# Performance work log

Hardware: AMD Instinct MI355X
Metric: run time of the kernel (lower is better)

## Reference

```python
import jax, jax.numpy as jnp
import numpy as np

N_NODES = 50000
N_EDGES = 800000
DIM = 128
N_LAYERS = 4
EPS = 1e-5  # BatchNorm1d default eps


def setup_inputs() -> dict:
    key = jax.random.key(0)
    k_x, k_e, k_w = jax.random.split(key, 3)
    x = jax.random.normal(k_x, (N_NODES, DIM), dtype=jnp.float32)
    edge_index = jax.random.randint(k_e, (2, N_EDGES), 0, N_NODES, dtype=jnp.int32)
    # stacked per-layer params (input_dim == hidden_dim == DIM)
    Ws = jax.random.normal(k_w, (N_LAYERS, DIM, DIM), dtype=jnp.float32) * (1.0 / np.sqrt(DIM))
    bs = jnp.zeros((N_LAYERS, DIM), jnp.float32)
    gammas = jnp.ones((N_LAYERS, DIM), jnp.float32)
    betas = jnp.zeros((N_LAYERS, DIM), jnp.float32)
    return {"x": x, "edge_index": edge_index, "Ws": Ws, "bs": bs,
            "gammas": gammas, "betas": betas}


def gcn_conv(x, W, b, src, dst, n):
    # PyG GCNConv: h = X W; out = D^{-1/2}(A+I)D^{-1/2} h + b
    h = x @ W                                       # [N, D]
    deg = jnp.zeros((n,), h.dtype).at[dst].add(1.0) + 1.0  # +1 self-loop
    dis = jax.lax.rsqrt(deg)                        # deg > 0 due to self-loops
    msg = h[src] * (dis[src] * dis[dst])[:, None]   # [E, D] gather + scale
    out = jnp.zeros_like(h).at[dst].add(msg)        # scatter-add aggregate
    out = out + h * (dis * dis)[:, None]            # self-loop term, norm = 1/deg
    return out + b


def batchnorm(z, gamma, beta):
    # BatchNorm1d training-mode math: batch mean, biased variance
    mu = z.mean(axis=0)
    var = z.var(axis=0)
    return (z - mu) * jax.lax.rsqrt(var + EPS) * gamma + beta


def reference(x, edge_index, Ws, bs, gammas, betas):
    src, dst = edge_index[0], edge_index[1]
    z = x
    for i in range(N_LAYERS):
        z = gcn_conv(z, Ws[i], bs[i], src, dst, z.shape[0])
        z = jax.nn.relu(z)
        z = batchnorm(z, gammas[i], betas[i])
        # Dropout: identity (eval mode / deterministic reference)
    return z
```

## Files before the change

### kernel.cpp

```cpp
#include <hip/hip_runtime.h>

#define N_NODES 50000
#define N_EDGES 800000
#define DIM 128
#define NLAYERS 4
#define BN_EPS 1e-5f
#define SCAN_BLOCKS 196
#define WS2 72

typedef __attribute__((ext_vector_type(8))) short short8;
typedef __attribute__((ext_vector_type(4))) float f32x4;

__device__ __forceinline__ float bf2f(unsigned short u){
    union { unsigned int i; float f; } x; x.i = ((unsigned int)u) << 16; return x.f;
}
__device__ __forceinline__ unsigned short f2bf(float f){
    union { float f; unsigned int i; } x; x.f = f;
    unsigned int lsb = (x.i >> 16) & 1u;
    unsigned int r = x.i + 0x7fffu + lsb;
    return (unsigned short)(r >> 16);
}

struct P4 { int2 a, b, c, d; };

__device__ __forceinline__ P4 loadP_mask(const int2* __restrict__ ep, int base,
                                         int sub, int lim){
    P4 p;
    int i0 = base + sub, i1 = base + 4 + sub, i2 = base + 8 + sub, i3 = base + 12 + sub;
    p.a = (i0 < lim) ? ep[i0] : make_int2(0, 0);
    p.b = (i1 < lim) ? ep[i1] : make_int2(0, 0);
    p.c = (i2 < lim) ? ep[i2] : make_int2(0, 0);
    p.d = (i3 < lim) ? ep[i3] : make_int2(0, 0);
    return p;
}
__device__ __forceinline__ P4 loadP_full(const int2* __restrict__ ep, int base,
                                         int sub){
    P4 p;
    p.a = ep[base + sub];
    p.b = ep[base + 4 + sub];
    p.c = ep[base + 8 + sub];
    p.d = ep[base + 12 + sub];
    return p;
}
__device__ __forceinline__ P4 loadP(const int2* __restrict__ ep, int base,
                                    int sub, int lim){
    if (lim - base >= 16) return loadP_full(ep, base, sub);
    return loadP_mask(ep, base, sub, lim);
}


__global__ __launch_bounds__(256) void k_zero(int* __restrict__ p, int n){
    int i = blockIdx.x * 256 + threadIdx.x;
    if (i < n) p[i] = 0;
}

__global__ __launch_bounds__(256) void k_count(const int* __restrict__ dst,
                                               int* __restrict__ degcnt){
    int e = blockIdx.x * 256 + threadIdx.x;
    if (e < N_EDGES) atomicAdd(&degcnt[dst[e]], 1);
}

__global__ __launch_bounds__(256) void k_scan1(const int* __restrict__ degcnt,
                                               int* __restrict__ rowptr,
                                               int* __restrict__ bsum,
                                               float* __restrict__ dis){
    __shared__ int tmp[256];
    int t = threadIdx.x;
    int i = blockIdx.x * 256 + t;
    int v = (i < N_NODES) ? degcnt[i] : 0;
    if (i < N_NODES) dis[i] = rsqrtf((float)v + 1.0f);
    tmp[t] = v;
    __syncthreads();
    #pragma unroll
    for (int off = 1; off < 256; off <<= 1){
        int u = (t >= off) ? tmp[t - off] : 0;
        __syncthreads();
        tmp[t] += u;
        __syncthreads();
    }
    if (i < N_NODES) rowptr[i] = tmp[t] - v;
    if (t == 255) bsum[blockIdx.x] = tmp[255];
}

__global__ __launch_bounds__(256) void k_scan3(const int* __restrict__ bsum,
                                               int* __restrict__ rowptr,
                                               int* __restrict__ wptr){
    __shared__ int tmp[256];
    int t = threadIdx.x;
    int v = (t < SCAN_BLOCKS) ? bsum[t] : 0;
    tmp[t] = v;
    __syncthreads();
    #pragma unroll
    for (int off = 1; off < 256; off <<= 1){
        int u = (t >= off) ? tmp[t - off] : 0;
        __syncthreads();
        tmp[t] += u;
        __syncthreads();
    }
    int boff = (blockIdx.x == 0) ? 0 : tmp[blockIdx.x - 1];
    int i = blockIdx.x * 256 + t;
    if (i < N_NODES){
        int r = rowptr[i] + boff;
        rowptr[i] = r; wptr[i] = r;
    }
    if (i == 0) rowptr[N_NODES] = N_EDGES;
}

__global__ __launch_bounds__(256) void k_fill(const int* __restrict__ src,
                                              const int* __restrict__ dst,
                                              const float* __restrict__ dis,
                                              int* __restrict__ wptr,
                                              int2* __restrict__ epair){
    int e = blockIdx.x * 256 + threadIdx.x;
    if (e < N_EDGES){
        int s = src[e], d = dst[e];
        float w = dis[s] * dis[d];
        int p = atomicAdd(&wptr[d], 1);
        int2 pr; pr.x = s; pr.y = __float_as_int(w);
        epair[p] = pr;
    }
}


template<int MODE>
__global__ __launch_bounds__(256) void k_gemm(const void* __restrict__ zraw,
                                              const float* __restrict__ W,
                                              const float* __restrict__ stats,
                                              const float* __restrict__ gamma,
                                              const float* __restrict__ beta,
                                              unsigned short* __restrict__ hb){
    __shared__ short whi[DIM * WS2];
    __shared__ short wlo[DIM * WS2];
    __shared__ float scs[DIM], shs[DIM];
    __shared__ float part[256];
    __shared__ float b2[DIM];
    int tid = threadIdx.x;

    if (MODE == 1){
        if (tid < DIM){
            float mu  = stats[tid] * (1.0f / N_NODES);
            float var = stats[DIM + tid] * (1.0f / N_NODES) - mu * mu;
            float sc  = rsqrtf(var + BN_EPS) * gamma[tid];
            scs[tid] = sc;
            shs[tid] = beta[tid] - mu * sc;
        }
        __syncthreads();
        {
            int c = tid >> 1, half = tid & 1;
            float acc = 0.f;
            int k0 = half * 64;
            #pragma unroll 4
            for (int k = k0; k < k0 + 64; k++)
                acc = fmaf(shs[k], W[k*DIM + c], acc);
            part[tid] = acc;
        }
    } else {
        if (tid < DIM) b2[tid] = 0.f;
    }

    int lane = tid & 63;
    int wv   = tid >> 6;
    int m = lane & 15;
    int q = lane >> 4;
    int row0 = blockIdx.x * 64 + wv * 16;
    int arow = row0 + m;
    bool avalid = arow < N_NODES;

    f32x4 acc[8];
    #pragma unroll
    for (int t = 0; t < 8; t++) acc[t] = (f32x4){0.f, 0.f, 0.f, 0.f};

    #pragma unroll
    for (int half = 0; half < 2; half++){
        #pragma unroll
        for (int it = 0; it < 4; it++){
            int ch = tid + 256*it;
            int kc = ch >> 7, c = ch & 127;
            int kbase = half*64 + kc*8;
            short8 vh, vl;
            #pragma unroll
            for (int i = 0; i < 8; i++){
                float v = W[(kbase + i)*DIM + c];
                if (MODE == 1) v *= scs[kbase + i];
                unsigned short h = f2bf(v);
                float lo = v - bf2f(h);
                vh[i] = (short)h;
                vl[i] = (short)f2bf(lo);
            }
            *(short8*)&whi[c*WS2 + kc*8] = vh;
            *(short8*)&wlo[c*WS2 + kc*8] = vl;
        }
        __syncthreads();
        if (MODE == 1 && half == 0){
            if (tid < DIM) b2[tid] = part[2*tid] + part[2*tid + 1];
        }

        #pragma unroll
        for (int gl2 = 0; gl2 < 2; gl2++){
            int gg = half*2 + gl2;
            short8 a = {0,0,0,0,0,0,0,0};
            if (avalid){
                if (MODE == 0){
                    const float* xp = (const float*)zraw + (size_t)arow*DIM + gg*32 + q*8;
                    float4 v0 = *(const float4*)xp;
                    float4 v1 = *(const float4*)(xp + 4);
                    a[0] = (short)f2bf(v0.x); a[1] = (short)f2bf(v0.y);
                    a[2] = (short)f2bf(v0.z); a[3] = (short)f2bf(v0.w);
                    a[4] = (short)f2bf(v1.x); a[5] = (short)f2bf(v1.y);
                    a[6] = (short)f2bf(v1.z); a[7] = (short)f2bf(v1.w);
                } else {
                    a = *(const short8*)((const unsigned short*)zraw
                          + (size_t)gg*N_NODES*32 + (size_t)arow*32 + q*8);
                }
            }
            #pragma unroll
            for (int t = 0; t < 8; t++){
                int col = t*16 + m;
                int off = col*WS2 + gl2*32 + q*8;
                short8 bh = *(const short8*)&whi[off];
                short8 bl = *(const short8*)&wlo[off];
                acc[t] = __builtin_amdgcn_mfma_f32_16x16x32_bf16(a, bh, acc[t], 0, 0, 0);
                acc[t] = __builtin_amdgcn_mfma_f32_16x16x32_bf16(a, bl, acc[t], 0, 0, 0);
            }
        }
        if (half == 0) __syncthreads();
    }

    #pragma unroll
    for (int t = 0; t < 8; t++){
        int colg = t*16 + m;
        float bz = b2[colg];
        size_t base = (size_t)(t >> 1)*N_NODES*32 + (t & 1)*16 + m;
        #pragma unroll
        for (int r = 0; r < 4; r++){
            int row = row0 + q*4 + r;
            if (row < N_NODES)
                hb[base + (size_t)row*32] = f2bf(acc[t][r] + bz);
        }
    }
}

__global__ __launch_bounds__(256) void k_agg(const unsigned short* __restrict__ h,
                                             const int* __restrict__ rowptr,
                                             const int2* __restrict__ epair,
                                             const float* __restrict__ dis,
                                             const float* __restrict__ bias,
                                             unsigned short* __restrict__ out,
                                             float* __restrict__ stats){
    int lane = threadIdx.x & 63;
    int w    = threadIdx.x >> 6;
    int g    = blockIdx.x & 3;
    int sub  = lane >> 4;
    int cp   = lane & 15;
    const ushort2* hg = (const ushort2*)(h + (size_t)g * N_NODES * 32);
    ushort2* og = (ushort2*)(out + (size_t)g * N_NODES * 32);
    float b0 = bias[g*32 + 2*cp], b1 = bias[g*32 + 2*cp + 1];
    float s0 = 0.f, s1 = 0.f, q0 = 0.f, q1 = 0.f;
    int bg = blockIdx.x >> 2;
    int nstride = (gridDim.x >> 2) * 4;

    int node = bg*4 + w;
    int ne0 = 0, ne1 = 0;
    ushort2 nhv; nhv.x = 0; nhv.y = 0;
    float ndi = 0.f;
    P4 nP = {{0,0},{0,0},{0,0},{0,0}};
    if (node < N_NODES){
        ne0 = rowptr[node];
        ne1 = rowptr[node + 1];
        nhv = hg[node*16 + cp];
        ndi = dis[node];
        nP  = loadP(epair, ne0, sub, ne1);
    }

    while (node < N_NODES){
        int e0 = ne0, e1 = ne1;
        ushort2 hv = nhv;
        float di = ndi;
        P4 P = nP;

        int nnext = node + nstride;
        if (nnext < N_NODES){
            ne0 = rowptr[nnext];
            ne1 = rowptr[nnext + 1];
            nhv = hg[nnext*16 + cp];
            ndi = dis[nnext];
        } else { ne0 = 0; ne1 = 0; }

        float pa0 = 0.f, pa1 = 0.f, pb0 = 0.f, pb1 = 0.f;
        float pc0 = 0.f, pc1 = 0.f, pd0 = 0.f, pd1 = 0.f;
        if (sub == 0){
            float dii = di * di;
            pa0 = bf2f(hv.x) * dii; pa1 = bf2f(hv.y) * dii;
        }

        int e = e0;
        while (e < e1){
            int en = e + 16;
            P4 Pn = {{0,0},{0,0},{0,0},{0,0}};
            if (en < e1) Pn = loadP(epair, en, sub, e1);
            ushort2 X0 = hg[P.a.x*16 + cp];
            ushort2 X1 = hg[P.b.x*16 + cp];
            ushort2 X2 = hg[P.c.x*16 + cp];
            ushort2 X3 = hg[P.d.x*16 + cp];
            float w0 = __int_as_float(P.a.y), w1 = __int_as_float(P.b.y);
            float w2 = __int_as_float(P.c.y), w3 = __int_as_float(P.d.y);
            pa0 = fmaf(bf2f(X0.x), w0, pa0); pa1 = fmaf(bf2f(X0.y), w0, pa1);
            pb0 = fmaf(bf2f(X1.x), w1, pb0); pb1 = fmaf(bf2f(X1.y), w1, pb1);
            pc0 = fmaf(bf2f(X2.x), w2, pc0); pc1 = fmaf(bf2f(X2.y), w2, pc1);
            pd0 = fmaf(bf2f(X3.x), w3, pd0); pd1 = fmaf(bf2f(X3.y), w3, pd1);
            P = Pn;
            e = en;
        }

        float r0 = (pa0 + pb0) + (pc0 + pd0);
        float r1 = (pa1 + pb1) + (pc1 + pd1);
        r0 += __shfl_xor(r0, 16); r1 += __shfl_xor(r1, 16);
        r0 += __shfl_xor(r0, 32); r1 += __shfl_xor(r1, 32);
        if (sub == 0){
            float a0 = fmaxf(r0 + b0, 0.f);
            float a1 = fmaxf(r1 + b1, 0.f);
            ushort2 ov; ov.x = f2bf(a0); ov.y = f2bf(a1);
            og[node*16 + cp] = ov;
            s0 += a0; s1 += a1; q0 += a0*a0; q1 += a1*a1;
        }

        if (nnext < N_NODES)
            nP = loadP(epair, ne0, sub, ne1);
        node = nnext;
    }

    __shared__ float red[4][16][4];
    if (sub == 0){
        red[w][cp][0] = s0; red[w][cp][1] = s1;
        red[w][cp][2] = q0; red[w][cp][3] = q1;
    }
    __syncthreads();
    if (w == 0 && sub == 0){
        #pragma unroll
        for (int ww = 1; ww < 4; ww++){
            s0 += red[ww][cp][0]; s1 += red[ww][cp][1];
            q0 += red[ww][cp][2]; q1 += red[ww][cp][3];
        }
        int c = g*32 + 2*cp;
        atomicAdd(&stats[c],         s0);
        atomicAdd(&stats[c + 1],     s1);
        atomicAdd(&stats[DIM + c],     q0);
        atomicAdd(&stats[DIM + c + 1], q1);
    }
}

__global__ __launch_bounds__(256) void k_bn(const uint4* __restrict__ in,
                                            const float* __restrict__ stats,
                                            const float* __restrict__ gamma,
                                            const float* __restrict__ beta,
                                            float4* __restrict__ outf){
    __shared__ float scs[DIM], shs[DIM];
    int tid = threadIdx.x;
    if (tid < DIM){
        float mu  = stats[tid] * (1.0f / N_NODES);
        float var = stats[DIM + tid] * (1.0f / N_NODES) - mu * mu;
        float sc  = rsqrtf(var + BN_EPS) * gamma[tid];
        scs[tid] = sc;
        shs[tid] = beta[tid] - mu * sc;
    }
    __syncthreads();

    int i = blockIdx.x * 256 + tid;
    if (i >= N_NODES * DIM / 8) return;
    int row = i >> 4;
    int c = (i * 8) & (DIM - 1);
    int gg = c >> 5, wi = c & 31;
    uint4 raw = in[gg*(N_NODES*4) + row*4 + (wi >> 3)];
    unsigned int u[4] = {raw.x, raw.y, raw.z, raw.w};
    float v[8];
    #pragma unroll
    for (int j = 0; j < 4; j++){
        v[2*j]   = bf2f((unsigned short)(u[j] & 0xffff));
        v[2*j+1] = bf2f((unsigned short)(u[j] >> 16));
    }
    float4 r0, r1;
    r0.x = fmaf(v[0], scs[c+0], shs[c+0]);
    r0.y = fmaf(v[1], scs[c+1], shs[c+1]);
    r0.z = fmaf(v[2], scs[c+2], shs[c+2]);
    r0.w = fmaf(v[3], scs[c+3], shs[c+3]);
    r1.x = fmaf(v[4], scs[c+4], shs[c+4]);
    r1.y = fmaf(v[5], scs[c+5], shs[c+5]);
    r1.z = fmaf(v[6], scs[c+6], shs[c+6]);
    r1.w = fmaf(v[7], scs[c+7], shs[c+7]);
    outf[2*i]   = r0;
    outf[2*i+1] = r1;
}


extern "C" void kernel_launch(void* const* d_in, const int* in_sizes, int n_in,
                              void* d_out, int out_size, void* d_ws, size_t ws_size,
                              hipStream_t stream){
    const float* x   = (const float*)d_in[0];
    const int*   src = (const int*)d_in[1];
    const int*   dst = src + N_EDGES;
    const float* Ws  = (const float*)d_in[2];
    const float* bs  = (const float*)d_in[3];
    const float* gs  = (const float*)d_in[4];
    const float* be  = (const float*)d_in[5];

    char* w = (char*)d_ws;
    int*   degcnt = (int*)(w);
    float* stats  = (float*)(w + 200000);
    float* dis    = (float*)(w + 208192);
    int*   rowptr = (int*)(w + 408192);
    int*   wptr   = (int*)(w + 608208);
    int*   bsum   = (int*)(w + 808208);
    int2*  epair  = (int2*)(w + 875280);
    unsigned short* bufA = (unsigned short*)(w + 7275280);
    unsigned short* hb   = (unsigned short*)(w + 20075280);

    k_zero<<<(51024 + 255)/256, 256, 0, stream>>>(degcnt, 51024);
    k_count<<<3125, 256, 0, stream>>>(dst, degcnt);
    k_scan1<<<SCAN_BLOCKS, 256, 0, stream>>>(degcnt, rowptr, bsum, dis);
    k_scan3<<<SCAN_BLOCKS, 256, 0, stream>>>(bsum, rowptr, wptr);
    k_fill<<<3125, 256, 0, stream>>>(src, dst, dis, wptr, epair);

    for (int L = 0; L < NLAYERS; L++){
        const float* Wl = Ws + L*DIM*DIM;
        if (L == 0)
            k_gemm<0><<<(N_NODES + 63)/64, 256, 0, stream>>>(x, Wl,
                    nullptr, nullptr, nullptr, hb);
        else
            k_gemm<1><<<(N_NODES + 63)/64, 256, 0, stream>>>(bufA, Wl,
                    stats + (L-1)*256, gs + (L-1)*DIM, be + (L-1)*DIM, hb);
        k_agg<<<2048, 256, 0, stream>>>(hb, rowptr, epair, dis, bs + L*DIM,
                                        bufA, stats + L*256);
    }
    k_bn<<<3125, 256, 0, stream>>>((const uint4*)bufA, stats + 3*256,
                                   gs + 3*DIM, be + 3*DIM, (float4*)d_out);
}
```

Measured before the change: 552.8 us.

## Pack edge index and fp16 weight into 32 bits, nontemporal loads, more agg blocks

Each CSR edge entry is packed from an int2 (source index plus fp32 weight) into one 32-bit word holding a 16-bit source index and an fp16 normalization weight, halving edge-list traffic in the aggregation kernel. Edge loads and output stores now use nontemporal hints, and the aggregation grid doubles to 4096 blocks. The packing assumes node ids fit in 16 bits, but N_NODES is 50000, which is below 65536, so it holds. The fp16 weight adds some rounding error.

```diff
diff --git a/kernel.cpp b/kernel.cpp
--- a/kernel.cpp
+++ b/kernel.cpp
@@ -1,4 +1,5 @@
 #include <hip/hip_runtime.h>
+#include <hip/hip_fp16.h>
 
 #define N_NODES 50000
 #define N_EDGES 800000
@@ -20,32 +21,35 @@
     unsigned int r = x.i + 0x7fffu + lsb;
     return (unsigned short)(r >> 16);
 }
-
-struct P4 { int2 a, b, c, d; };
-
-__device__ __forceinline__ P4 loadP_mask(const int2* __restrict__ ep, int base,
+__device__ __forceinline__ float unpack_w(unsigned p){
+    return __half2float(__ushort_as_half((unsigned short)(p >> 16)));
+}
+
+struct U4 { unsigned a, b, c, d; };
+
+__device__ __forceinline__ U4 loadU_mask(const unsigned* __restrict__ ep, int base,
                                          int sub, int lim){
-    P4 p;
+    U4 p;
     int i0 = base + sub, i1 = base + 4 + sub, i2 = base + 8 + sub, i3 = base + 12 + sub;
-    p.a = (i0 < lim) ? ep[i0] : make_int2(0, 0);
-    p.b = (i1 < lim) ? ep[i1] : make_int2(0, 0);
-    p.c = (i2 < lim) ? ep[i2] : make_int2(0, 0);
-    p.d = (i3 < lim) ? ep[i3] : make_int2(0, 0);
+    p.a = (i0 < lim) ? __builtin_nontemporal_load(ep + i0) : 0u;
+    p.b = (i1 < lim) ? __builtin_nontemporal_load(ep + i1) : 0u;
+    p.c = (i2 < lim) ? __builtin_nontemporal_load(ep + i2) : 0u;
+    p.d = (i3 < lim) ? __builtin_nontemporal_load(ep + i3) : 0u;
     return p;
 }
-__device__ __forceinline__ P4 loadP_full(const int2* __restrict__ ep, int base,
+__device__ __forceinline__ U4 loadU_full(const unsigned* __restrict__ ep, int base,
                                          int sub){
-    P4 p;
-    p.a = ep[base + sub];
-    p.b = ep[base + 4 + sub];
-    p.c = ep[base + 8 + sub];
-    p.d = ep[base + 12 + sub];
+    U4 p;
+    p.a = __builtin_nontemporal_load(ep + base + sub);
+    p.b = __builtin_nontemporal_load(ep + base + 4 + sub);
+    p.c = __builtin_nontemporal_load(ep + base + 8 + sub);
+    p.d = __builtin_nontemporal_load(ep + base + 12 + sub);
     return p;
 }
-__device__ __forceinline__ P4 loadP(const int2* __restrict__ ep, int base,
+__device__ __forceinline__ U4 loadU(const unsigned* __restrict__ ep, int base,
                                     int sub, int lim){
-    if (lim - base >= 16) return loadP_full(ep, base, sub);
-    return loadP_mask(ep, base, sub, lim);
+    if (lim - base >= 16) return loadU_full(ep, base, sub);
+    return loadU_mask(ep, base, sub, lim);
 }
 
 
@@ -110,14 +114,14 @@
                                               const int* __restrict__ dst,
                                               const float* __restrict__ dis,
                                               int* __restrict__ wptr,
-                                              int2* __restrict__ epair){
+                                              unsigned* __restrict__ epk){
     int e = blockIdx.x * 256 + threadIdx.x;
     if (e < N_EDGES){
         int s = src[e], d = dst[e];
         float w = dis[s] * dis[d];
+        unsigned short wh = __half_as_ushort(__float2half(w));
         int p = atomicAdd(&wptr[d], 1);
-        int2 pr; pr.x = s; pr.y = __float_as_int(w);
-        epair[p] = pr;
+        epk[p] = ((unsigned)wh << 16) | (unsigned)s;
     }
 }
 
@@ -242,7 +246,7 @@
 
 __global__ __launch_bounds__(256) void k_agg(const unsigned short* __restrict__ h,
                                              const int* __restrict__ rowptr,
-                                             const int2* __restrict__ epair,
+                                             const unsigned* __restrict__ epk,
                                              const float* __restrict__ dis,
                                              const float* __restrict__ bias,
                                              unsigned short* __restrict__ out,
@@ -253,7 +257,7 @@
     int sub  = lane >> 4;
     int cp   = lane & 15;
     const ushort2* hg = (const ushort2*)(h + (size_t)g * N_NODES * 32);
-    ushort2* og = (ushort2*)(out + (size_t)g * N_NODES * 32);
+    unsigned* og = (unsigned*)(out + (size_t)g * N_NODES * 32);
     float b0 = bias[g*32 + 2*cp], b1 = bias[g*32 + 2*cp + 1];
     float s0 = 0.f, s1 = 0.f, q0 = 0.f, q1 = 0.f;
     int bg = blockIdx.x >> 2;
@@ -263,20 +267,20 @@
     int ne0 = 0, ne1 = 0;
     ushort2 nhv; nhv.x = 0; nhv.y = 0;
     float ndi = 0.f;
-    P4 nP = {{0,0},{0,0},{0,0},{0,0}};
+    U4 nP = {0u, 0u, 0u, 0u};
     if (node < N_NODES){
         ne0 = rowptr[node];
         ne1 = rowptr[node + 1];
         nhv = hg[node*16 + cp];
         ndi = dis[node];
-        nP  = loadP(epair, ne0, sub, ne1);
+        nP  = loadU(epk, ne0, sub, ne1);
     }
 
     while (node < N_NODES){
         int e0 = ne0, e1 = ne1;
         ushort2 hv = nhv;
         float di = ndi;
-        P4 P = nP;
+        U4 P = nP;
 
         int nnext = node + nstride;
         if (nnext < N_NODES){
@@ -296,14 +300,14 @@
         int e = e0;
         while (e < e1){
             int en = e + 16;
-            P4 Pn = {{0,0},{0,0},{0,0},{0,0}};
-            if (en < e1) Pn = loadP(epair, en, sub, e1);
-            ushort2 X0 = hg[P.a.x*16 + cp];
-            ushort2 X1 = hg[P.b.x*16 + cp];
-            ushort2 X2 = hg[P.c.x*16 + cp];
-            ushort2 X3 = hg[P.d.x*16 + cp];
-            float w0 = __int_as_float(P.a.y), w1 = __int_as_float(P.b.y);
-            float w2 = __int_as_float(P.c.y), w3 = __int_as_float(P.d.y);
+            U4 Pn = {0u, 0u, 0u, 0u};
+            if (en < e1) Pn = loadU(epk, en, sub, e1);
+            ushort2 X0 = hg[(P.a & 0xffff)*16 + cp];
+            ushort2 X1 = hg[(P.b & 0xffff)*16 + cp];
+            ushort2 X2 = hg[(P.c & 0xffff)*16 + cp];
+            ushort2 X3 = hg[(P.d & 0xffff)*16 + cp];
+            float w0 = unpack_w(P.a), w1 = unpack_w(P.b);
+            float w2 = unpack_w(P.c), w3 = unpack_w(P.d);
             pa0 = fmaf(bf2f(X0.x), w0, pa0); pa1 = fmaf(bf2f(X0.y), w0, pa1);
             pb0 = fmaf(bf2f(X1.x), w1, pb0); pb1 = fmaf(bf2f(X1.y), w1, pb1);
             pc0 = fmaf(bf2f(X2.x), w2, pc0); pc1 = fmaf(bf2f(X2.y), w2, pc1);
@@ -319,13 +323,13 @@
         if (sub == 0){
             float a0 = fmaxf(r0 + b0, 0.f);
             float a1 = fmaxf(r1 + b1, 0.f);
-            ushort2 ov; ov.x = f2bf(a0); ov.y = f2bf(a1);
-            og[node*16 + cp] = ov;
+            unsigned ov = ((unsigned)f2bf(a1) << 16) | (unsigned)f2bf(a0);
+            __builtin_nontemporal_store(ov, og + node*16 + cp);
             s0 += a0; s1 += a1; q0 += a0*a0; q1 += a1*a1;
         }
 
         if (nnext < N_NODES)
-            nP = loadP(epair, ne0, sub, ne1);
+            nP = loadU(epk, ne0, sub, ne1);
         node = nnext;
     }
 
@@ -410,7 +414,7 @@
     int*   rowptr = (int*)(w + 408192);
     int*   wptr   = (int*)(w + 608208);
     int*   bsum   = (int*)(w + 808208);
-    int2*  epair  = (int2*)(w + 875280);
+    unsigned* epk = (unsigned*)(w + 875280);
     unsigned short* bufA = (unsigned short*)(w + 7275280);
     unsigned short* hb   = (unsigned short*)(w + 20075280);
 
@@ -418,7 +422,7 @@
     k_count<<<3125, 256, 0, stream>>>(dst, degcnt);
     k_scan1<<<SCAN_BLOCKS, 256, 0, stream>>>(degcnt, rowptr, bsum, dis);
     k_scan3<<<SCAN_BLOCKS, 256, 0, stream>>>(bsum, rowptr, wptr);
-    k_fill<<<3125, 256, 0, stream>>>(src, dst, dis, wptr, epair);
+    k_fill<<<3125, 256, 0, stream>>>(src, dst, dis, wptr, epk);
 
     for (int L = 0; L < NLAYERS; L++){
         const float* Wl = Ws + L*DIM*DIM;
@@ -428,7 +432,7 @@
         else
             k_gemm<1><<<(N_NODES + 63)/64, 256, 0, stream>>>(bufA, Wl,
                     stats + (L-1)*256, gs + (L-1)*DIM, be + (L-1)*DIM, hb);
-        k_agg<<<2048, 256, 0, stream>>>(hb, rowptr, epair, dis, bs + L*DIM,
+        k_agg<<<4096, 256, 0, stream>>>(hb, rowptr, epk, dis, bs + L*DIM,
                                         bufA, stats + L*256);
     }
     k_bn<<<3125, 256, 0, stream>>>((const uint4*)bufA, stats + 3*256,
```

After: 601.6 us. +8.8%, slower.
